# Kernel optimization log

Measured on AMD Instinct MI355X. Metric: run time of the kernel, lower is better.

Reference implementation:

```python
import jax, jax.numpy as jnp
import numpy as np

N_NODES = 100000
HID = 128
N_LAYERS = 3
N_EDGES = 1600000
EPS = 1e-5


def setup_inputs() -> dict:
    key = jax.random.key(0)
    ks = jax.random.split(key, 10)
    H, L = HID, N_LAYERS
    # edge_index: row 0 = src, row 1 = dst (PyG source_to_target flow)
    edge_index = jax.random.randint(ks[0], (2, N_EDGES), 0, N_NODES, dtype=jnp.int32)
    # xavier-uniform embedding
    lim = float(np.sqrt(6.0 / (N_NODES + H)))
    emb = jax.random.uniform(ks[1], (N_NODES, H), jnp.float32, -lim, lim)
    s = 1.0 / np.sqrt(H)
    Wl = jax.random.uniform(ks[2], (L, H, H), jnp.float32, -s, s)  # lin_l (neighbors), has bias
    bl = jax.random.uniform(ks[3], (L, H), jnp.float32, -s, s)
    Wr = jax.random.uniform(ks[4], (L, H, H), jnp.float32, -s, s)  # lin_r (root), no bias
    ln_gamma = jnp.ones((L, H), jnp.float32)
    ln_beta = jnp.zeros((L, H), jnp.float32)
    sj = 1.0 / np.sqrt(H * (L + 1))
    jkW = jax.random.uniform(ks[5], (H, H * (L + 1)), jnp.float32, -sj, sj)
    jkb = jax.random.uniform(ks[6], (H,), jnp.float32, -sj, sj)
    return {"emb": emb, "Wl": Wl, "bl": bl, "Wr": Wr,
            "ln_gamma": ln_gamma, "ln_beta": ln_beta,
            "jkW": jkW, "jkb": jkb, "edge_index": edge_index}


def _layernorm(x, gamma, beta):
    mu = jnp.mean(x, axis=-1, keepdims=True)
    var = jnp.mean(jnp.square(x - mu), axis=-1, keepdims=True)
    return (x - mu) * jax.lax.rsqrt(var + EPS) * gamma + beta


def reference(emb, Wl, bl, Wr, ln_gamma, ln_beta, jkW, jkb, edge_index):
    src, dst = edge_index[0], edge_index[1]
    n = emb.shape[0]
    # in-degree for mean aggregation (clamped to avoid div-by-zero)
    deg = jax.ops.segment_sum(jnp.ones_like(dst, dtype=emb.dtype), dst, num_segments=n)
    inv_deg = (1.0 / jnp.maximum(deg, 1.0))[:, None]
    x = emb
    xs = [x]
    for i in range(N_LAYERS):
        x_prev = x
        # scatter-mean of neighbor features (gather [E,H] -> segment_sum [N,H])
        agg = jax.ops.segment_sum(x[src], dst, num_segments=n) * inv_deg
        # SAGEConv: lin_l(agg) + lin_r(x)
        x = agg @ Wl[i].T + bl[i] + x @ Wr[i].T
        x = _layernorm(x, ln_gamma[i], ln_beta[i])
        x = jax.nn.relu(x)
        # dropout is identity in eval mode
        if i > 0:
            x = x + x_prev
        xs.append(x)
    # jumping-knowledge concat + projection
    x = jnp.concatenate(xs, axis=1) @ jkW.T + jkb
    return x
```

## Files before the change

### kernel.cpp

```cpp
#include <hip/hip_runtime.h>
#include <hip/hip_bf16.h>
#include <stdint.h>

#define HID 128
#define BSHIFT 7
#define NBLK 64

typedef __attribute__((ext_vector_type(8))) __bf16 bf16x8;
typedef __attribute__((ext_vector_type(4))) float f32x4;
typedef __attribute__((ext_vector_type(2))) float f32x2;

static __device__ __forceinline__ float bf2f(ushort h){
  union { uint u; float f; } c; c.u = ((uint)h) << 16; return c.f;
}
static __device__ __forceinline__ float u2f(uint u){
  union { uint u; float f; } c; c.u = u; return c.f;
}
static __device__ __forceinline__ ushort f2bf(float f){
  union { float f; uint u; } c; c.f = f;
  uint u = c.u;
  return (ushort)((u + 0x7fffu + ((u >> 16) & 1u)) >> 16);
}
static __device__ __forceinline__ bf16x8 load8(const ushort* p){
  return *(const bf16x8*)p;
}

__global__ void k_cvt(const float* __restrict__ in, ushort* __restrict__ out, int n){
  int i = blockIdx.x * 256 + threadIdx.x;
  if (i < n) out[i] = f2bf(in[i]);
}

__global__ void k_cvtw(const float* __restrict__ Wl, const float* __restrict__ Wr,
                       ushort* __restrict__ outF, int total){
  int o = blockIdx.x * 256 + threadIdx.x;
  if (o >= total) return;
  int layer = o >> 15;
  int r = o & 32767;
  int e    = r & 7;
  int lane = (r >> 3) & 63;
  int jt   = (r >> 9) & 7;
  int mat  = (r >> 12) & 1;
  int kt   = r >> 13;
  int l16 = lane & 15, quad = lane >> 4;
  int j = l16 * 8 + jt;
  int k = kt * 32 + quad * 8 + e;
  const float* W = mat ? Wr : Wl;
  outF[o] = f2bf(W[layer * 16384 + j * 128 + k]);
}

__global__ void k_cvtjk(const float* __restrict__ jkW, ushort* __restrict__ outF){
  int o = blockIdx.x * 256 + threadIdx.x;
  int e    = o & 7;
  int lane = (o >> 3) & 63;
  int jt   = (o >> 9) & 7;
  int kt   = o >> 12;
  int l16 = lane & 15, quad = lane >> 4;
  int j = l16 * 4 + (jt & 3) + (jt >> 2) * 64;
  int k = kt * 32 + quad * 8 + e;
  outF[o] = f2bf(jkW[j * 512 + k]);
}

__global__ __launch_bounds__(1024) void k_count(
    const int* __restrict__ dst, int* __restrict__ rowcnt, int E, int NB, int es){
  __shared__ int h[1024];
  int blk = blockIdx.x;
  for (int i = threadIdx.x; i < NB; i += 1024) h[i] = 0;
  __syncthreads();
  int e0 = blk * es, e1 = min(e0 + es, E);
  for (int e = e0 + threadIdx.x; e < e1; e += 1024)
    atomicAdd(&h[dst[e] >> BSHIFT], 1);
  __syncthreads();
  for (int i = threadIdx.x; i < NB; i += 1024)
    rowcnt[blk * NB + i] = h[i];
}

__global__ __launch_bounds__(1024) void k_colscan(
    int* __restrict__ rowcnt, int* __restrict__ bbase, int NB, int nblk){
  int b = threadIdx.x;
  int total = 0;
  if (b < NB)
    for (int r = 0; r < nblk; r++) total += rowcnt[r * NB + b];
  int lane = b & 63, w = b >> 6;
  int x = total;
  #pragma unroll
  for (int d = 1; d < 64; d <<= 1){ int y = __shfl_up(x, d, 64); if (lane >= d) x += y; }
  __shared__ int tmp[16];
  if (lane == 63) tmp[w] = x;
  __syncthreads();
  if (b < 64){
    int s = (lane < 16) ? tmp[lane] : 0;
    #pragma unroll
    for (int d = 1; d < 16; d <<= 1){ int y = __shfl_up(s, d, 64); if (lane >= d) s += y; }
    if (lane < 16) tmp[lane] = s;
  }
  __syncthreads();
  int base = ((w > 0) ? tmp[w - 1] : 0) + x - total;
  if (b < NB){
    bbase[b] = base;
    int acc = base;
    for (int r = 0; r < nblk; r++){
      int v = rowcnt[r * NB + b];
      rowcnt[r * NB + b] = acc;
      acc += v;
    }
    if (b == NB - 1) bbase[NB] = acc;
  }
}

__global__ __launch_bounds__(1024) void k_place(
    const int* __restrict__ src, const int* __restrict__ dst,
    const int* __restrict__ rowcnt, uint* __restrict__ binned, int E, int NB, int es){
  __shared__ int cur[1024];
  int blk = blockIdx.x;
  for (int i = threadIdx.x; i < NB; i += 1024) cur[i] = rowcnt[blk * NB + i];
  __syncthreads();
  int e0 = blk * es, e1 = min(e0 + es, E);
  for (int e = e0 + threadIdx.x; e < e1; e += 1024){
    int d = dst[e];
    int b = d >> BSHIFT;
    int pos = atomicAdd(&cur[b], 1);
    binned[pos] = ((uint)src[e] << BSHIFT) | (uint)(d & 127);
  }
}

__global__ __launch_bounds__(256) void k_bpass(
    const uint* __restrict__ binned, const int* __restrict__ bbase,
    int* __restrict__ csr, int* __restrict__ offs, int* __restrict__ cnt, int N){
  int b = blockIdx.x;
  int n0 = b << BSHIFT;
  int tid = threadIdx.x;
  __shared__ int lcnt[128], loffs[128];
  if (tid < 128) lcnt[tid] = 0;
  __syncthreads();
  int base = bbase[b];
  int m = bbase[b + 1] - base;
  const uint* bp = binned + base;
  uint vv[12]; int slot[12];
  #pragma unroll
  for (int u = 0; u < 12; u++){
    int i = tid + u * 256;
    if (i < m){
      uint v = bp[i];
      vv[u] = v;
      slot[u] = atomicAdd(&lcnt[v & 127], 1);
    }
  }
  __syncthreads();
  if (tid < 64){
    int a0 = lcnt[tid * 2], a1 = lcnt[tid * 2 + 1];
    int s = a0 + a1;
    int x = s;
    #pragma unroll
    for (int d = 1; d < 64; d <<= 1){ int y = __shfl_up(x, d, 64); if (tid >= d) x += y; }
    int excl = x - s;
    loffs[tid * 2] = excl;
    loffs[tid * 2 + 1] = excl + a0;
  }
  __syncthreads();
  if (tid < 128 && n0 + tid < N){
    cnt[n0 + tid] = lcnt[tid];
    offs[n0 + tid] = base + loffs[tid];
  }
  #pragma unroll
  for (int u = 0; u < 12; u++){
    int i = tid + u * 256;
    if (i < m){
      uint v = vv[u];
      csr[base + loffs[v & 127] + slot[u]] = (int)(v >> BSHIFT);
    }
  }
}

__global__ __launch_bounds__(256) void k_aggregate(
    const ushort* __restrict__ x, const int* __restrict__ csr,
    const int* __restrict__ offs, const int* __restrict__ cnt,
    ushort* __restrict__ agg, int N){
  int node = blockIdx.x * 4 + (threadIdx.x >> 6);
  int lane = threadIdx.x & 63;
  if (node >= N) return;
  int half = lane >> 5;
  int l32  = lane & 31;
  uint lb  = (uint)(l32 << 3);
  int beg = offs[node], d = cnt[node];
  if (d == 0){
    if (half == 0){
      uint2 z = {0u, 0u};
      *(uint2*)(agg + (size_t)node * HID + l32 * 4) = z;
    }
    return;
  }
  const int* __restrict__ cp = csr + beg;
  const char* __restrict__ xb = (const char*)x;
  f32x2 sx = {0.f, 0.f}, sy = {0.f, 0.f};
  int i = 0;
  for (; i + 16 <= d; i += 16){
    uint off[8];
    #pragma unroll
    for (int u = 0; u < 8; u++)
      off[u] = ((uint)cp[i + 2 * u + half] << 8) + lb;
    uint2 v[8];
    #pragma unroll
    for (int u = 0; u < 8; u++)
      v[u] = *(const uint2*)(xb + off[u]);
    #pragma unroll
    for (int u = 0; u < 8; u++){
      f32x2 tx = { u2f(v[u].x << 16), u2f(v[u].x & 0xffff0000u) };
      f32x2 ty = { u2f(v[u].y << 16), u2f(v[u].y & 0xffff0000u) };
      sx += tx; sy += ty;
    }
  }
  if (i < d){
    uint off[8]; bool ok[8];
    #pragma unroll
    for (int u = 0; u < 8; u++){
      int pos = i + 2 * u + half;
      ok[u] = pos < d;
      off[u] = ((uint)cp[ok[u] ? pos : d - 1] << 8) + lb;
    }
    uint2 v[8];
    #pragma unroll
    for (int u = 0; u < 8; u++)
      v[u] = *(const uint2*)(xb + off[u]);
    #pragma unroll
    for (int u = 0; u < 8; u++){
      uint ax = ok[u] ? v[u].x : 0u;
      uint ay = ok[u] ? v[u].y : 0u;
      f32x2 tx = { u2f(ax << 16), u2f(ax & 0xffff0000u) };
      f32x2 ty = { u2f(ay << 16), u2f(ay & 0xffff0000u) };
      sx += tx; sy += ty;
    }
  }
  sx.x += __shfl_xor(sx.x, 32, 64);
  sx.y += __shfl_xor(sx.y, 32, 64);
  sy.x += __shfl_xor(sy.x, 32, 64);
  sy.y += __shfl_xor(sy.y, 32, 64);
  if (half == 0){
    float inv = 1.0f / fmaxf((float)d, 1.0f);
    uint2 o;
    o.x = (uint)f2bf(sx.x * inv) | ((uint)f2bf(sx.y * inv) << 16);
    o.y = (uint)f2bf(sy.x * inv) | ((uint)f2bf(sy.y * inv) << 16);
    *(uint2*)(agg + (size_t)node * HID + l32 * 4) = o;
  }
}

template<int HAS_RES>
__global__ __launch_bounds__(256, 4) void k_layer(
    const ushort* __restrict__ agg, const ushort* __restrict__ xin,
    const ushort* __restrict__ Wf,
    const float* __restrict__ bl, const float* __restrict__ gamma,
    const float* __restrict__ beta,
    ushort* __restrict__ xout, int N){
  int tid = threadIdx.x;
  int wv = tid >> 6, lane = tid & 63;
  int quad = lane >> 4, l16 = lane & 15;
  int rowbase = blockIdx.x * 128 + wv * 32;
  int r0 = rowbase + l16;      if (r0 >= N) r0 = N - 1;
  int r1 = rowbase + 16 + l16; if (r1 >= N) r1 = N - 1;
  int aq = quad * 8;

  const ushort* pa0 = agg + (size_t)r0 * HID;
  const ushort* pa1 = agg + (size_t)r1 * HID;
  const ushort* px0 = xin + (size_t)r0 * HID;
  const ushort* px1 = xin + (size_t)r1 * HID;

  f32x4 acc[2][8];
  {
    float4 bi0 = *(const float4*)(bl + l16 * 8);
    float4 bi1 = *(const float4*)(bl + l16 * 8 + 4);
    float bia[8] = {bi0.x, bi0.y, bi0.z, bi0.w, bi1.x, bi1.y, bi1.z, bi1.w};
    #pragma unroll
    for (int jt = 0; jt < 8; jt++){
      float b = bia[jt];
      f32x4 c = {b, b, b, b};
      acc[0][jt] = c; acc[1][jt] = c;
    }
  }

  bf16x8 c0 = load8(pa0 + aq), c1 = load8(pa1 + aq);
  bf16x8 c2 = load8(px0 + aq), c3 = load8(px1 + aq);
  #pragma unroll
  for (int kt = 0; kt < 4; kt++){
    bf16x8 n0 = c0, n1 = c1, n2 = c2, n3 = c3;
    if (kt < 3){
      int ao = (kt + 1) * 32 + aq;
      n0 = load8(pa0 + ao); n1 = load8(pa1 + ao);
      n2 = load8(px0 + ao); n3 = load8(px1 + ao);
    }
    #pragma unroll
    for (int jt = 0; jt < 8; jt++){
      bf16x8 bL = load8(Wf + ((kt * 16 + jt) * 64 + lane) * 8);
      bf16x8 bR = load8(Wf + ((kt * 16 + 8 + jt) * 64 + lane) * 8);
      acc[0][jt] = __builtin_amdgcn_mfma_f32_16x16x32_bf16(c0, bL, acc[0][jt], 0, 0, 0);
      acc[1][jt] = __builtin_amdgcn_mfma_f32_16x16x32_bf16(c1, bL, acc[1][jt], 0, 0, 0);
      acc[0][jt] = __builtin_amdgcn_mfma_f32_16x16x32_bf16(c2, bR, acc[0][jt], 0, 0, 0);
      acc[1][jt] = __builtin_amdgcn_mfma_f32_16x16x32_bf16(c3, bR, acc[1][jt], 0, 0, 0);
    }
    c0 = n0; c1 = n1; c2 = n2; c3 = n3;
  }

  float4 g0 = *(const float4*)(gamma + l16 * 8);
  float4 g1 = *(const float4*)(gamma + l16 * 8 + 4);
  float4 be0 = *(const float4*)(beta + l16 * 8);
  float4 be1 = *(const float4*)(beta + l16 * 8 + 4);
  float gg[8] = {g0.x, g0.y, g0.z, g0.w, g1.x, g1.y, g1.z, g1.w};
  float bb[8] = {be0.x, be0.y, be0.z, be0.w, be1.x, be1.y, be1.z, be1.w};

  #pragma unroll
  for (int rt = 0; rt < 2; rt++){
    float s1[4] = {0,0,0,0}, s2[4] = {0,0,0,0};
    #pragma unroll
    for (int jt = 0; jt < 8; jt++){
      #pragma unroll
      for (int r = 0; r < 4; r++){ float v = acc[rt][jt][r]; s1[r] += v; s2[r] += v * v; }
    }
    #pragma unroll
    for (int m = 1; m < 16; m <<= 1){
      #pragma unroll
      for (int r = 0; r < 4; r++){
        s1[r] += __shfl_xor(s1[r], m, 64);
        s2[r] += __shfl_xor(s2[r], m, 64);
      }
    }
    #pragma unroll
    for (int r = 0; r < 4; r++){
      float mu = s1[r] * (1.f / 128.f);
      float var = s2[r] * (1.f / 128.f) - mu * mu;
      float rs = rsqrtf(var + 1e-5f);
      int row = rowbase + rt * 16 + quad * 4 + r;
      int rowc = row < N ? row : N - 1;
      uint rw[4] = {0u, 0u, 0u, 0u};
      if (HAS_RES){
        uint4 rv = *(const uint4*)(xin + (size_t)rowc * HID + l16 * 8);
        rw[0] = rv.x; rw[1] = rv.y; rw[2] = rv.z; rw[3] = rv.w;
      }
      uint ow[4];
      #pragma unroll
      for (int p = 0; p < 4; p++){
        float v0 = (acc[rt][2 * p][r] - mu) * rs * gg[2 * p] + bb[2 * p];
        float v1 = (acc[rt][2 * p + 1][r] - mu) * rs * gg[2 * p + 1] + bb[2 * p + 1];
        v0 = fmaxf(v0, 0.f);
        v1 = fmaxf(v1, 0.f);
        if (HAS_RES){
          v0 += bf2f((ushort)(rw[p] & 0xffffu));
          v1 += bf2f((ushort)(rw[p] >> 16));
        }
        ow[p] = (uint)f2bf(v0) | ((uint)f2bf(v1) << 16);
      }
      uint4 o;
      o.x = ow[0]; o.y = ow[1]; o.z = ow[2]; o.w = ow[3];
      if (row < N)
        *(uint4*)(xout + (size_t)row * HID + l16 * 8) = o;
    }
  }
}

__global__ __launch_bounds__(256, 4) void k_jk(
    const ushort* __restrict__ emb, const ushort* __restrict__ x1,
    const ushort* __restrict__ x2, const ushort* __restrict__ x3,
    const ushort* __restrict__ Wf,
    const float* __restrict__ jkb, float* __restrict__ out, int N){
  int tid = threadIdx.x;
  int wv = tid >> 6, lane = tid & 63;
  int quad = lane >> 4, l16 = lane & 15;
  int rowbase = blockIdx.x * 128 + wv * 32;
  int r0 = rowbase + l16;      if (r0 >= N) r0 = N - 1;
  int r1 = rowbase + 16 + l16; if (r1 >= N) r1 = N - 1;
  int aq = quad * 8;
  size_t o0 = (size_t)r0 * HID, o1 = (size_t)r1 * HID;

  f32x4 acc[2][8];
  #pragma unroll
  for (int jt = 0; jt < 8; jt++){
    f32x4 z = {0.f, 0.f, 0.f, 0.f};
    acc[0][jt] = z; acc[1][jt] = z;
  }

  const ushort* srcs[4] = {emb, x1, x2, x3};
  bf16x8 a0 = load8(emb + o0 + aq);
  bf16x8 a1 = load8(emb + o1 + aq);
  #pragma unroll
  for (int ktg = 0; ktg < 16; ktg++){
    bf16x8 n0 = a0, n1 = a1;
    if (ktg < 15){
      const ushort* sp = srcs[(ktg + 1) >> 2];
      int ao = ((ktg + 1) & 3) * 32 + aq;
      n0 = load8(sp + o0 + ao);
      n1 = load8(sp + o1 + ao);
    }
    #pragma unroll
    for (int jt = 0; jt < 8; jt++){
      bf16x8 bW = load8(Wf + ((ktg * 8 + jt) * 64 + lane) * 8);
      acc[0][jt] = __builtin_amdgcn_mfma_f32_16x16x32_bf16(a0, bW, acc[0][jt], 0, 0, 0);
      acc[1][jt] = __builtin_amdgcn_mfma_f32_16x16x32_bf16(a1, bW, acc[1][jt], 0, 0, 0);
    }
    a0 = n0; a1 = n1;
  }

  float4 jb0 = *(const float4*)(jkb + l16 * 4);
  float4 jb1 = *(const float4*)(jkb + 64 + l16 * 4);
  float bia[8] = {jb0.x, jb0.y, jb0.z, jb0.w, jb1.x, jb1.y, jb1.z, jb1.w};

  #pragma unroll
  for (int rt = 0; rt < 2; rt++){
    #pragma unroll
    for (int r = 0; r < 4; r++){
      int row = rowbase + rt * 16 + quad * 4 + r;
      if (row < N){
        f32x4 v0 = {acc[rt][0][r] + bia[0], acc[rt][1][r] + bia[1],
                    acc[rt][2][r] + bia[2], acc[rt][3][r] + bia[3]};
        f32x4 v1 = {acc[rt][4][r] + bia[4], acc[rt][5][r] + bia[5],
                    acc[rt][6][r] + bia[6], acc[rt][7][r] + bia[7]};
        *(f32x4*)(out + (size_t)row * HID + l16 * 4) = v0;
        *(f32x4*)(out + (size_t)row * HID + 64 + l16 * 4) = v1;
      }
    }
  }
}

extern "C" void kernel_launch(void* const* d_in, const int* in_sizes, int n_in,
                              void* d_out, int out_size, void* d_ws, size_t ws_size,
                              hipStream_t stream){
  const float* emb   = (const float*)d_in[0];
  const float* Wl    = (const float*)d_in[1];
  const float* bl    = (const float*)d_in[2];
  const float* Wr    = (const float*)d_in[3];
  const float* gamma = (const float*)d_in[4];
  const float* beta  = (const float*)d_in[5];
  const float* jkW   = (const float*)d_in[6];
  const float* jkb   = (const float*)d_in[7];
  const int*   eidx  = (const int*)d_in[8];
  int N = in_sizes[0] / HID;
  int E = in_sizes[8] / 2;
  const int* src = eidx;
  const int* dst = eidx + E;
  float* out = (float*)d_out;

  int NB = (N + 127) >> BSHIFT;
  int es = (E + NBLK - 1) / NBLK;

  char* w = (char*)d_ws;
  auto carve = [&](size_t bytes) -> char* {
    char* p = w; w += (bytes + 255) & ~(size_t)255; return p;
  };
  int Npad = ((N + 127) / 128) * 128;
  int* rowcnt   = (int*)carve((size_t)NBLK * NB * 4);
  int* bbase    = (int*)carve((size_t)(NB + 1) * 4);
  uint* binned  = (uint*)carve((size_t)E * 4);
  int* cnt      = (int*)carve((size_t)N * 4);
  int* offs     = (int*)carve((size_t)N * 4);
  int* csr      = (int*)carve((size_t)E * 4);
  ushort* Wfrag = (ushort*)carve((size_t)3 * 32768 * 2);
  ushort* jkWf  = (ushort*)carve((size_t)65536 * 2);
  ushort* embbf = (ushort*)carve((size_t)Npad * HID * 2);
  ushort* agg   = (ushort*)carve((size_t)Npad * HID * 2);
  ushort* x1    = (ushort*)carve((size_t)Npad * HID * 2);
  ushort* x2    = (ushort*)carve((size_t)Npad * HID * 2);
  ushort* x3    = (ushort*)carve((size_t)Npad * HID * 2);

  int nEmb = N * HID;
  k_cvtw<<<(3 * 32768 + 255) / 256, 256, 0, stream>>>(Wl, Wr, Wfrag, 3 * 32768);
  k_cvtjk<<<65536 / 256, 256, 0, stream>>>(jkW, jkWf);
  k_cvt<<<(nEmb + 255) / 256, 256, 0, stream>>>(emb, embbf, nEmb);

  k_count<<<NBLK, 1024, 0, stream>>>(dst, rowcnt, E, NB, es);
  k_colscan<<<1, 1024, 0, stream>>>(rowcnt, bbase, NB, NBLK);
  k_place<<<NBLK, 1024, 0, stream>>>(src, dst, rowcnt, binned, E, NB, es);
  k_bpass<<<NB, 256, 0, stream>>>(binned, bbase, csr, offs, cnt, N);

  int aggBlocks = (N + 3) / 4;
  int gemmBlocks = (N + 127) / 128;

  k_aggregate<<<aggBlocks, 256, 0, stream>>>(embbf, csr, offs, cnt, agg, N);
  k_layer<0><<<gemmBlocks, 256, 0, stream>>>(agg, embbf, Wfrag, bl, gamma, beta, x1, N);
  k_aggregate<<<aggBlocks, 256, 0, stream>>>(x1, csr, offs, cnt, agg, N);
  k_layer<1><<<gemmBlocks, 256, 0, stream>>>(agg, x1, Wfrag + 32768, bl + HID,
                                             gamma + HID, beta + HID, x2, N);
  k_aggregate<<<aggBlocks, 256, 0, stream>>>(x2, csr, offs, cnt, agg, N);
  k_layer<1><<<gemmBlocks, 256, 0, stream>>>(agg, x2, Wfrag + 2 * 32768, bl + 2 * HID,
                                             gamma + 2 * HID, beta + 2 * HID, x3, N);
  k_jk<<<gemmBlocks, 256, 0, stream>>>(embbf, x1, x2, x3, jkWf, jkb, out, N);
}
```

Before: 519.2 us.

## Fuse neighbor aggregation into SAGE layer kernel via swizzled LDS staging

The separate scatter-mean aggregation kernel is merged into the per-layer GEMM/LayerNorm kernel. Each wave gathers and averages neighbor features for its own 32 rows and writes them into XOR-swizzled shared memory. The MFMA loop then reads the aggregated A operand from LDS instead of a global agg buffer. This removes the global write and read of the aggregation tensor and three kernel launches. The cost is far fewer waves in flight during the latency-bound gather, since each wave now processes 32 nodes serially, plus 32KB of LDS per block.

```diff
diff --git a/kernel.cpp b/kernel.cpp
--- a/kernel.cpp
+++ b/kernel.cpp
@@ -171,97 +171,108 @@
   }
 }
 
-__global__ __launch_bounds__(256) void k_aggregate(
-    const ushort* __restrict__ x, const int* __restrict__ csr,
-    const int* __restrict__ offs, const int* __restrict__ cnt,
-    ushort* __restrict__ agg, int N){
-  int node = blockIdx.x * 4 + (threadIdx.x >> 6);
-  int lane = threadIdx.x & 63;
-  if (node >= N) return;
-  int half = lane >> 5;
-  int l32  = lane & 31;
-  uint lb  = (uint)(l32 << 3);
-  int beg = offs[node], d = cnt[node];
-  if (d == 0){
-    if (half == 0){
-      uint2 z = {0u, 0u};
-      *(uint2*)(agg + (size_t)node * HID + l32 * 4) = z;
-    }
-    return;
-  }
-  const int* __restrict__ cp = csr + beg;
-  const char* __restrict__ xb = (const char*)x;
-  f32x2 sx = {0.f, 0.f}, sy = {0.f, 0.f};
-  int i = 0;
-  for (; i + 16 <= d; i += 16){
-    uint off[8];
-    #pragma unroll
-    for (int u = 0; u < 8; u++)
-      off[u] = ((uint)cp[i + 2 * u + half] << 8) + lb;
-    uint2 v[8];
-    #pragma unroll
-    for (int u = 0; u < 8; u++)
-      v[u] = *(const uint2*)(xb + off[u]);
-    #pragma unroll
-    for (int u = 0; u < 8; u++){
-      f32x2 tx = { u2f(v[u].x << 16), u2f(v[u].x & 0xffff0000u) };
-      f32x2 ty = { u2f(v[u].y << 16), u2f(v[u].y & 0xffff0000u) };
-      sx += tx; sy += ty;
-    }
-  }
-  if (i < d){
-    uint off[8]; bool ok[8];
-    #pragma unroll
-    for (int u = 0; u < 8; u++){
-      int pos = i + 2 * u + half;
-      ok[u] = pos < d;
-      off[u] = ((uint)cp[ok[u] ? pos : d - 1] << 8) + lb;
-    }
-    uint2 v[8];
-    #pragma unroll
-    for (int u = 0; u < 8; u++)
-      v[u] = *(const uint2*)(xb + off[u]);
-    #pragma unroll
-    for (int u = 0; u < 8; u++){
-      uint ax = ok[u] ? v[u].x : 0u;
-      uint ay = ok[u] ? v[u].y : 0u;
-      f32x2 tx = { u2f(ax << 16), u2f(ax & 0xffff0000u) };
-      f32x2 ty = { u2f(ay << 16), u2f(ay & 0xffff0000u) };
-      sx += tx; sy += ty;
-    }
-  }
-  sx.x += __shfl_xor(sx.x, 32, 64);
-  sx.y += __shfl_xor(sx.y, 32, 64);
-  sy.x += __shfl_xor(sy.x, 32, 64);
-  sy.y += __shfl_xor(sy.y, 32, 64);
-  if (half == 0){
-    float inv = 1.0f / fmaxf((float)d, 1.0f);
-    uint2 o;
-    o.x = (uint)f2bf(sx.x * inv) | ((uint)f2bf(sx.y * inv) << 16);
-    o.y = (uint)f2bf(sy.x * inv) | ((uint)f2bf(sy.y * inv) << 16);
-    *(uint2*)(agg + (size_t)node * HID + l32 * 4) = o;
-  }
-}
-
 template<int HAS_RES>
-__global__ __launch_bounds__(256, 4) void k_layer(
-    const ushort* __restrict__ agg, const ushort* __restrict__ xin,
+__global__ __launch_bounds__(256, 4) void k_agglayer(
+    const ushort* __restrict__ xin,
+    const int* __restrict__ csr, const int* __restrict__ offs,
+    const int* __restrict__ cnt,
     const ushort* __restrict__ Wf,
     const float* __restrict__ bl, const float* __restrict__ gamma,
     const float* __restrict__ beta,
     ushort* __restrict__ xout, int N){
+  __shared__ ushort sA[16384];
   int tid = threadIdx.x;
   int wv = tid >> 6, lane = tid & 63;
   int quad = lane >> 4, l16 = lane & 15;
-  int rowbase = blockIdx.x * 128 + wv * 32;
-  int r0 = rowbase + l16;      if (r0 >= N) r0 = N - 1;
-  int r1 = rowbase + 16 + l16; if (r1 >= N) r1 = N - 1;
+  int rowbase = blockIdx.x * 128;
+  int nbase = rowbase + wv * 32;
+
+  int nl = lane & 31;
+  int nn = nbase + nl;
+  bool nv = nn < N;
+  int o32 = offs[nv ? nn : 0];
+  int c32 = nv ? cnt[nn] : 0;
+
+  int half = lane >> 5;
+  uint lb = (uint)(nl << 3);
+  const char* __restrict__ xb = (const char*)xin;
+  char* __restrict__ sAb = (char*)sA;
+
+  for (int j = 0; j < 32; j++){
+    int beg = __shfl(o32, j, 64);
+    int d   = __shfl(c32, j, 64);
+    int lr = wv * 32 + j;
+    uint wo = (uint)(lr << 8) + (lb ^ (uint)((lr & 7) << 4));
+    if (d == 0){
+      if (half == 0){ uint2 z = {0u, 0u}; *(uint2*)(sAb + wo) = z; }
+      continue;
+    }
+    const int* __restrict__ cp = csr + beg;
+    f32x2 sx = {0.f, 0.f}, sy = {0.f, 0.f};
+    int i = 0;
+    for (; i + 16 <= d; i += 16){
+      uint off[8];
+      #pragma unroll
+      for (int u = 0; u < 8; u++)
+        off[u] = ((uint)cp[i + 2 * u + half] << 8) + lb;
+      uint2 v[8];
+      #pragma unroll
+      for (int u = 0; u < 8; u++)
+        v[u] = *(const uint2*)(xb + off[u]);
+      #pragma unroll
+      for (int u = 0; u < 8; u++){
+        f32x2 tx = { u2f(v[u].x << 16), u2f(v[u].x & 0xffff0000u) };
+        f32x2 ty = { u2f(v[u].y << 16), u2f(v[u].y & 0xffff0000u) };
+        sx += tx; sy += ty;
+      }
+    }
+    if (i < d){
+      uint off[8]; bool ok[8];
+      #pragma unroll
+      for (int u = 0; u < 8; u++){
+        int pos = i + 2 * u + half;
+        ok[u] = pos < d;
+        off[u] = ((uint)cp[ok[u] ? pos : d - 1] << 8) + lb;
+      }
+      uint2 v[8];
+      #pragma unroll
+      for (int u = 0; u < 8; u++)
+        v[u] = *(const uint2*)(xb + off[u]);
+      #pragma unroll
+      for (int u = 0; u < 8; u++){
+        uint ax = ok[u] ? v[u].x : 0u;
+        uint ay = ok[u] ? v[u].y : 0u;
+        f32x2 tx = { u2f(ax << 16), u2f(ax & 0xffff0000u) };
+        f32x2 ty = { u2f(ay << 16), u2f(ay & 0xffff0000u) };
+        sx += tx; sy += ty;
+      }
+    }
+    sx.x += __shfl_xor(sx.x, 32, 64);
+    sx.y += __shfl_xor(sx.y, 32, 64);
+    sy.x += __shfl_xor(sy.x, 32, 64);
+    sy.y += __shfl_xor(sy.y, 32, 64);
+    if (half == 0){
+      float inv = 1.0f / fmaxf((float)d, 1.0f);
+      uint2 o;
+      o.x = (uint)f2bf(sx.x * inv) | ((uint)f2bf(sx.y * inv) << 16);
+      o.y = (uint)f2bf(sy.x * inv) | ((uint)f2bf(sy.y * inv) << 16);
+      *(uint2*)(sAb + wo) = o;
+    }
+  }
+
+  int wrow = rowbase + wv * 32;
+  int r0 = wrow + l16;      if (r0 >= N) r0 = N - 1;
+  int r1 = wrow + 16 + l16; if (r1 >= N) r1 = N - 1;
   int aq = quad * 8;
-
-  const ushort* pa0 = agg + (size_t)r0 * HID;
-  const ushort* pa1 = agg + (size_t)r1 * HID;
   const ushort* px0 = xin + (size_t)r0 * HID;
   const ushort* px1 = xin + (size_t)r1 * HID;
+
+  bf16x8 xr0[4], xr1[4];
+  #pragma unroll
+  for (int kt = 0; kt < 4; kt++){
+    xr0[kt] = load8(px0 + aq + kt * 32);
+    xr1[kt] = load8(px1 + aq + kt * 32);
+  }
 
   f32x4 acc[2][8];
   {
@@ -276,26 +287,23 @@
     }
   }
 
-  bf16x8 c0 = load8(pa0 + aq), c1 = load8(pa1 + aq);
-  bf16x8 c2 = load8(px0 + aq), c3 = load8(px1 + aq);
+  int lr0 = wv * 32 + l16, lr1 = lr0 + 16;
   #pragma unroll
   for (int kt = 0; kt < 4; kt++){
-    bf16x8 n0 = c0, n1 = c1, n2 = c2, n3 = c3;
-    if (kt < 3){
-      int ao = (kt + 1) * 32 + aq;
-      n0 = load8(pa0 + ao); n1 = load8(pa1 + ao);
-      n2 = load8(px0 + ao); n3 = load8(px1 + ao);
-    }
+    uint bo = (uint)(kt * 64 + quad * 16);
+    uint a0 = (uint)(lr0 << 8) + (bo ^ (uint)((lr0 & 7) << 4));
+    uint a1 = (uint)(lr1 << 8) + (bo ^ (uint)((lr1 & 7) << 4));
+    bf16x8 aL0 = *(const bf16x8*)(sAb + a0);
+    bf16x8 aL1 = *(const bf16x8*)(sAb + a1);
     #pragma unroll
     for (int jt = 0; jt < 8; jt++){
       bf16x8 bL = load8(Wf + ((kt * 16 + jt) * 64 + lane) * 8);
       bf16x8 bR = load8(Wf + ((kt * 16 + 8 + jt) * 64 + lane) * 8);
-      acc[0][jt] = __builtin_amdgcn_mfma_f32_16x16x32_bf16(c0, bL, acc[0][jt], 0, 0, 0);
-      acc[1][jt] = __builtin_amdgcn_mfma_f32_16x16x32_bf16(c1, bL, acc[1][jt], 0, 0, 0);
-      acc[0][jt] = __builtin_amdgcn_mfma_f32_16x16x32_bf16(c2, bR, acc[0][jt], 0, 0, 0);
-      acc[1][jt] = __builtin_amdgcn_mfma_f32_16x16x32_bf16(c3, bR, acc[1][jt], 0, 0, 0);
-    }
-    c0 = n0; c1 = n1; c2 = n2; c3 = n3;
+      acc[0][jt] = __builtin_amdgcn_mfma_f32_16x16x32_bf16(aL0, bL, acc[0][jt], 0, 0, 0);
+      acc[1][jt] = __builtin_amdgcn_mfma_f32_16x16x32_bf16(aL1, bL, acc[1][jt], 0, 0, 0);
+      acc[0][jt] = __builtin_amdgcn_mfma_f32_16x16x32_bf16(xr0[kt], bR, acc[0][jt], 0, 0, 0);
+      acc[1][jt] = __builtin_amdgcn_mfma_f32_16x16x32_bf16(xr1[kt], bR, acc[1][jt], 0, 0, 0);
+    }
   }
 
   float4 g0 = *(const float4*)(gamma + l16 * 8);
@@ -326,7 +334,7 @@
       float mu = s1[r] * (1.f / 128.f);
       float var = s2[r] * (1.f / 128.f) - mu * mu;
       float rs = rsqrtf(var + 1e-5f);
-      int row = rowbase + rt * 16 + quad * 4 + r;
+      int row = wrow + rt * 16 + quad * 4 + r;
       int rowc = row < N ? row : N - 1;
       uint rw[4] = {0u, 0u, 0u, 0u};
       if (HAS_RES){
@@ -452,7 +460,6 @@
   ushort* Wfrag = (ushort*)carve((size_t)3 * 32768 * 2);
   ushort* jkWf  = (ushort*)carve((size_t)65536 * 2);
   ushort* embbf = (ushort*)carve((size_t)Npad * HID * 2);
-  ushort* agg   = (ushort*)carve((size_t)Npad * HID * 2);
   ushort* x1    = (ushort*)carve((size_t)Npad * HID * 2);
   ushort* x2    = (ushort*)carve((size_t)Npad * HID * 2);
   ushort* x3    = (ushort*)carve((size_t)Npad * HID * 2);
@@ -467,16 +474,13 @@
   k_place<<<NBLK, 1024, 0, stream>>>(src, dst, rowcnt, binned, E, NB, es);
   k_bpass<<<NB, 256, 0, stream>>>(binned, bbase, csr, offs, cnt, N);
 
-  int aggBlocks = (N + 3) / 4;
   int gemmBlocks = (N + 127) / 128;
 
-  k_aggregate<<<aggBlocks, 256, 0, stream>>>(embbf, csr, offs, cnt, agg, N);
-  k_layer<0><<<gemmBlocks, 256, 0, stream>>>(agg, embbf, Wfrag, bl, gamma, beta, x1, N);
-  k_aggregate<<<aggBlocks, 256, 0, stream>>>(x1, csr, offs, cnt, agg, N);
-  k_layer<1><<<gemmBlocks, 256, 0, stream>>>(agg, x1, Wfrag + 32768, bl + HID,
-                                             gamma + HID, beta + HID, x2, N);
-  k_aggregate<<<aggBlocks, 256, 0, stream>>>(x2, csr, offs, cnt, agg, N);
-  k_layer<1><<<gemmBlocks, 256, 0, stream>>>(agg, x2, Wfrag + 2 * 32768, bl + 2 * HID,
-                                             gamma + 2 * HID, beta + 2 * HID, x3, N);
+  k_agglayer<0><<<gemmBlocks, 256, 0, stream>>>(embbf, csr, offs, cnt,
+      Wfrag, bl, gamma, beta, x1, N);
+  k_agglayer<1><<<gemmBlocks, 256, 0, stream>>>(x1, csr, offs, cnt,
+      Wfrag + 32768, bl + HID, gamma + HID, beta + HID, x2, N);
+  k_agglayer<1><<<gemmBlocks, 256, 0, stream>>>(x2, csr, offs, cnt,
+      Wfrag + 2 * 32768, bl + 2 * HID, gamma + 2 * HID, beta + 2 * HID, x3, N);
   k_jk<<<gemmBlocks, 256, 0, stream>>>(embbf, x1, x2, x3, jkWf, jkb, out, N);
 }
```

New measurement: 530.9 us. 2.2% more time.
